# Kernel tuning notes

Hardware: AMD Instinct MI355X
Metric: run time of the kernel (lower is better)

The kernel has to match this reference:

```python
import jax, jax.numpy as jnp
import numpy as np

IN_DIM, EDGE_DIM, HID = 128, 64, 128
N_A, N_B, E_AB, E_AA = 50000, 50000, 320000, 320000


def setup_inputs() -> dict:
    key = jax.random.key(0)
    ks = jax.random.split(key, 13)
    inv = lambda n: 1.0 / np.sqrt(n)
    return {
        "x_a": jax.random.normal(ks[0], (N_A, IN_DIM), jnp.float32),
        "x_b": jax.random.normal(ks[1], (N_B, IN_DIM), jnp.float32),
        "ei_ab": jax.random.randint(ks[2], (2, E_AB), 0, N_A),
        "ea_ab": jax.random.normal(ks[3], (E_AB, EDGE_DIM), jnp.float32),
        "ei_aa": jax.random.randint(ks[4], (2, E_AA), 0, N_A),
        "ea_aa": jax.random.normal(ks[5], (E_AA, EDGE_DIM), jnp.float32),
        "Wh_w": jax.random.normal(ks[6], (EDGE_DIM, HID), jnp.float32) * inv(EDGE_DIM),
        "Wh_b": jnp.zeros((HID,), jnp.float32),
        "Wn_w": jax.random.normal(ks[7], (2 * IN_DIM, HID), jnp.float32) * inv(2 * IN_DIM),
        "Wn_b": jnp.zeros((HID,), jnp.float32),
        "w_e": jax.random.normal(ks[8], (HID,), jnp.float32) * inv(HID),
        "ft_w": jax.random.normal(ks[9], (IN_DIM, IN_DIM), jnp.float32) * inv(IN_DIM),
        "ft_b": jnp.zeros((IN_DIM,), jnp.float32),
    }


def reference(x_a, x_b, ei_ab, ea_ab, ei_aa, ea_aa,
              Wh_w, Wh_b, Wn_w, Wn_b, w_e, ft_w, ft_b):
    def edge_alpha(x_src, x_dst, ei, ea):
        # gather src/dst feats -> linear + relu -> score -> softmax over all edges
        s, d = ei[0], ei[1]
        nf = jnp.concatenate([x_src[s], x_dst[d]], axis=1)          # [E, 2*in_dim]
        h = jax.nn.relu(ea @ Wh_w + Wh_b + nf @ Wn_w + Wn_b)         # [E, hid]
        return jax.nn.softmax(h @ w_e, axis=0)                       # [E]

    alpha_ab = edge_alpha(x_a, x_b, ei_ab, ea_ab)
    alpha_aa = edge_alpha(x_a, x_a, ei_aa, ea_aa)

    lf_a = jnp.zeros_like(x_a)
    lf_b = jnp.zeros_like(x_b)
    s_ab, d_ab = ei_ab[0], ei_ab[1]
    # cross-type edge: scatter into both endpoint node types
    lf_a = lf_a.at[s_ab].add(-alpha_ab[:, None] * x_b[d_ab])
    lf_b = lf_b.at[d_ab].add(-alpha_ab[:, None] * x_a[s_ab])
    s_aa, d_aa = ei_aa[0], ei_aa[1]
    # same-type edge: single scatter (src side only, per original)
    lf_a = lf_a.at[s_aa].add(-alpha_aa[:, None] * x_a[d_aa])

    out_a = x_a + lf_a
    out_a = out_a + (out_a @ ft_w + ft_b)
    out_b = x_b + lf_b
    out_b = out_b + (out_b @ ft_w + ft_b)
    return out_a, out_b, alpha_ab, alpha_aa
```

## Files before the change

### kernel.cpp

```cpp
#include <hip/hip_runtime.h>
#include <hip/hip_fp16.h>
#include <cstdint>
#include <cstddef>

#define N_A   50000
#define N_B   50000
#define E_AB  320000
#define E_AA  320000
#define IN_DIM 128
#define HID    128
#define ED     64

using bf16x8 = __attribute__((ext_vector_type(8))) short;
using f32x4  = __attribute__((ext_vector_type(4))) float;
typedef unsigned short ushort_t;
typedef unsigned int   uint_t;

__device__ inline ushort_t bf16r(float f) {
    uint_t u = __float_as_uint(f);
    u = (u + 0x7FFF + ((u >> 16) & 1)) >> 16;
    return (ushort_t)u;
}
__device__ inline float bf2f(ushort_t h) {
    return __uint_as_float(((uint_t)h) << 16);
}
__device__ inline ushort_t f16r(float f) { return __half_as_ushort(__float2half_rn(f)); }
__device__ inline float f16f(ushort_t u) { return __half2float(__ushort_as_half(u)); }
__device__ inline uint_t packh2(float a, float b) {
    return (uint_t)f16r(a) | ((uint_t)f16r(b) << 16);
}

__device__ inline void online_merge(float& m, float& l, float om, float ol) {
    const float nm = fmaxf(m, om);
    l = l * __expf(m - nm) + ol * __expf(om - nm);
    m = nm;
}

__global__ __launch_bounds__(64) void prep_w_all(
    const float* __restrict__ Wh, const float* __restrict__ W1,
    const float* __restrict__ W2, const float* __restrict__ FT,
    const float* __restrict__ we,
    ushort_t* __restrict__ BhWh, ushort_t* __restrict__ BlWh,
    ushort_t* __restrict__ BhW1, ushort_t* __restrict__ BlW1,
    ushort_t* __restrict__ BhW2, ushort_t* __restrict__ BlW2,
    ushort_t* __restrict__ BhFT, ushort_t* __restrict__ BlFT,
    float* __restrict__ wep)
{
    const int f = blockIdx.x;
    const int lane = threadIdx.x;
    if (f == 112) {
#pragma unroll
        for (int q = 0; q < 2; ++q) {
            const int idx = lane + q * 64;
            const int l15 = idx >> 3, ct = idx & 7;
            wep[idx] = we[ct * 16 + l15];
        }
        return;
    }
    const float* W; ushort_t *oh, *ol; int KT, fl;
    if (f < 16)      { W = Wh; oh = BhWh; ol = BlWh; KT = 2; fl = f; }
    else if (f < 48) { W = W1; oh = BhW1; ol = BlW1; KT = 4; fl = f - 16; }
    else if (f < 80) { W = W2; oh = BhW2; ol = BlW2; KT = 4; fl = f - 48; }
    else             { W = FT; oh = BhFT; ol = BlFT; KT = 4; fl = f - 80; }
    const int ct = fl / KT, kt = fl % KT;
    const int col = ct * 16 + (lane & 15);
    const int kb  = kt * 32 + (lane >> 4) * 8;
#pragma unroll
    for (int j = 0; j < 8; ++j) {
        const float v = W[(kb + j) * 128 + col];
        const ushort_t h = bf16r(v);
        oh[(size_t)(fl * 64 + lane) * 8 + j] = h;
        ol[(size_t)(fl * 64 + lane) * 8 + j] = bf16r(v - bf2f(h));
    }
}

__global__ __launch_bounds__(256) void proj_dual_mfma(
    const float* __restrict__ X,
    const ushort_t* __restrict__ B1h, const ushort_t* __restrict__ B1l,
    const ushort_t* __restrict__ B2h, const ushort_t* __restrict__ B2l,
    const float* __restrict__ bh, const float* __restrict__ bn,
    ushort_t* __restrict__ P1, ushort_t* __restrict__ P2,
    ushort_t* __restrict__ X16, int N)
{
    const int lane = threadIdx.x & 63;
    const int l15 = lane & 15, lg = lane >> 4;
    const int r0 = blockIdx.x * 64 + (threadIdx.x >> 6) * 16;
    const int arow = (r0 + l15 < N) ? (r0 + l15) : (N - 1);

    bf16x8 ahi[4], alo[4];
#pragma unroll
    for (int kt = 0; kt < 4; ++kt) {
        float v[8];
        *(float4*)(v + 0) = *(const float4*)&X[(size_t)arow * 128 + kt * 32 + lg * 8];
        *(float4*)(v + 4) = *(const float4*)&X[(size_t)arow * 128 + kt * 32 + lg * 8 + 4];
        uint4 xu;
        xu.x = packh2(v[0], v[1]); xu.y = packh2(v[2], v[3]);
        xu.z = packh2(v[4], v[5]); xu.w = packh2(v[6], v[7]);
        *(uint4*)&X16[(size_t)arow * 128 + kt * 32 + lg * 8] = xu;
#pragma unroll
        for (int j = 0; j < 8; ++j) {
            const ushort_t h = bf16r(v[j]);
            ahi[kt][j] = (short)h;
            alo[kt][j] = (short)bf16r(v[j] - bf2f(h));
        }
    }

    f32x4 acc1[8], acc2[8];
#pragma unroll
    for (int ct = 0; ct < 8; ++ct) {
        const float b = bh[ct * 16 + l15] + bn[ct * 16 + l15];
        acc1[ct] = (f32x4){b, b, b, b};
        acc2[ct] = (f32x4){0.f, 0.f, 0.f, 0.f};
    }

#pragma unroll
    for (int ct = 0; ct < 8; ++ct) {
#pragma unroll
        for (int kt = 0; kt < 4; ++kt) {
            const size_t fo = (size_t)((ct * 4 + kt) * 64 + lane) * 8;
            const bf16x8 b1h = *(const bf16x8*)&B1h[fo];
            const bf16x8 b1l = *(const bf16x8*)&B1l[fo];
            const bf16x8 b2h = *(const bf16x8*)&B2h[fo];
            const bf16x8 b2l = *(const bf16x8*)&B2l[fo];
            acc1[ct] = __builtin_amdgcn_mfma_f32_16x16x32_bf16(ahi[kt], b1h, acc1[ct], 0, 0, 0);
            acc1[ct] = __builtin_amdgcn_mfma_f32_16x16x32_bf16(alo[kt], b1h, acc1[ct], 0, 0, 0);
            acc1[ct] = __builtin_amdgcn_mfma_f32_16x16x32_bf16(ahi[kt], b1l, acc1[ct], 0, 0, 0);
            acc2[ct] = __builtin_amdgcn_mfma_f32_16x16x32_bf16(ahi[kt], b2h, acc2[ct], 0, 0, 0);
            acc2[ct] = __builtin_amdgcn_mfma_f32_16x16x32_bf16(alo[kt], b2h, acc2[ct], 0, 0, 0);
            acc2[ct] = __builtin_amdgcn_mfma_f32_16x16x32_bf16(ahi[kt], b2l, acc2[ct], 0, 0, 0);
        }
    }
#pragma unroll
    for (int i = 0; i < 4; ++i) {
        const int row = r0 + lg * 4 + i;
        if (row < N) {
            uint4 u1, u2;
            u1.x = packh2(acc1[0][i], acc1[1][i]); u1.y = packh2(acc1[2][i], acc1[3][i]);
            u1.z = packh2(acc1[4][i], acc1[5][i]); u1.w = packh2(acc1[6][i], acc1[7][i]);
            u2.x = packh2(acc2[0][i], acc2[1][i]); u2.y = packh2(acc2[2][i], acc2[3][i]);
            u2.z = packh2(acc2[4][i], acc2[5][i]); u2.w = packh2(acc2[6][i], acc2[7][i]);
            *(uint4*)&P1[(size_t)row * 128 + l15 * 8] = u1;
            *(uint4*)&P2[(size_t)row * 128 + l15 * 8] = u2;
        }
    }
}

__global__ __launch_bounds__(256) void proj_single_mfma(
    const float* __restrict__ X,
    const ushort_t* __restrict__ Bh, const ushort_t* __restrict__ Bl,
    ushort_t* __restrict__ P, ushort_t* __restrict__ X16, int N)
{
    const int lane = threadIdx.x & 63;
    const int l15 = lane & 15, lg = lane >> 4;
    const int r0 = blockIdx.x * 64 + (threadIdx.x >> 6) * 16;
    const int arow = (r0 + l15 < N) ? (r0 + l15) : (N - 1);

    bf16x8 ahi[4], alo[4];
#pragma unroll
    for (int kt = 0; kt < 4; ++kt) {
        float v[8];
        *(float4*)(v + 0) = *(const float4*)&X[(size_t)arow * 128 + kt * 32 + lg * 8];
        *(float4*)(v + 4) = *(const float4*)&X[(size_t)arow * 128 + kt * 32 + lg * 8 + 4];
        uint4 xu;
        xu.x = packh2(v[0], v[1]); xu.y = packh2(v[2], v[3]);
        xu.z = packh2(v[4], v[5]); xu.w = packh2(v[6], v[7]);
        *(uint4*)&X16[(size_t)arow * 128 + kt * 32 + lg * 8] = xu;
#pragma unroll
        for (int j = 0; j < 8; ++j) {
            const ushort_t h = bf16r(v[j]);
            ahi[kt][j] = (short)h;
            alo[kt][j] = (short)bf16r(v[j] - bf2f(h));
        }
    }

    f32x4 acc[8];
#pragma unroll
    for (int ct = 0; ct < 8; ++ct) acc[ct] = (f32x4){0.f, 0.f, 0.f, 0.f};

#pragma unroll
    for (int ct = 0; ct < 8; ++ct) {
#pragma unroll
        for (int kt = 0; kt < 4; ++kt) {
            const size_t fo = (size_t)((ct * 4 + kt) * 64 + lane) * 8;
            const bf16x8 bhf = *(const bf16x8*)&Bh[fo];
            const bf16x8 blf = *(const bf16x8*)&Bl[fo];
            acc[ct] = __builtin_amdgcn_mfma_f32_16x16x32_bf16(ahi[kt], bhf, acc[ct], 0, 0, 0);
            acc[ct] = __builtin_amdgcn_mfma_f32_16x16x32_bf16(alo[kt], bhf, acc[ct], 0, 0, 0);
            acc[ct] = __builtin_amdgcn_mfma_f32_16x16x32_bf16(ahi[kt], blf, acc[ct], 0, 0, 0);
        }
    }
#pragma unroll
    for (int i = 0; i < 4; ++i) {
        const int row = r0 + lg * 4 + i;
        if (row < N) {
            uint4 u;
            u.x = packh2(acc[0][i], acc[1][i]); u.y = packh2(acc[2][i], acc[3][i]);
            u.z = packh2(acc[4][i], acc[5][i]); u.w = packh2(acc[6][i], acc[7][i]);
            *(uint4*)&P[(size_t)row * 128 + l15 * 8] = u;
        }
    }
}

__global__ __launch_bounds__(512) void edge_score_k(
    const float* __restrict__ ea_ab, const float* __restrict__ ea_aa,
    const int*   __restrict__ ei_ab, const int*   __restrict__ ei_aa,
    const ushort_t* __restrict__ P1h,
    const ushort_t* __restrict__ P2ah, const ushort_t* __restrict__ P2bh,
    const ushort_t* __restrict__ Bhi,  const ushort_t* __restrict__ Blo,
    const float* __restrict__ wep,
    float* __restrict__ scAB, float* __restrict__ scAA,
    int* __restrict__ cntA, int* __restrict__ cntB,
    int* __restrict__ rkAab, int* __restrict__ rkBab, int* __restrict__ rkAaa,
    float* __restrict__ pm, float* __restrict__ pl)
{
    const int t    = threadIdx.x;
    const int lane = t & 63;
    const int l15  = lane & 15;
    const int lg   = lane >> 4;
    const int wv   = t >> 6;
    const int type = (blockIdx.x >= 2500);
    const int bb   = type ? (blockIdx.x - 2500) : blockIdx.x;
    const int eb   = bb * 128;

    const float* __restrict__ ea  = type ? ea_aa : ea_ab;
    const int*   __restrict__ ei  = type ? ei_aa : ei_ab;
    const ushort_t* __restrict__ P2h = type ? P2ah : P2bh;
    float* __restrict__ score = type ? scAA : scAB;

    __shared__ ushort_t sBh[8192];
    __shared__ ushort_t sBl[8192];
    {
        const uint4* gh = (const uint4*)Bhi;
        const uint4* gl = (const uint4*)Blo;
        uint4* sh = (uint4*)sBh;
        uint4* sl = (uint4*)sBl;
#pragma unroll
        for (int i = 0; i < 2; ++i) {
            sh[t + i * 512] = gh[t + i * 512];
            sl[t + i * 512] = gl[t + i * 512];
        }
    }

    if (t < 128) {
        const int e = eb + t;
        const int s = ei[e];
        const int r = atomicAdd(&cntA[s], 1);
        if (type) rkAaa[e] = r; else rkAab[e] = r;
    } else if (t < 256 && !type) {
        const int e = eb + (t - 128);
        const int d = ei[(size_t)E_AB + e];
        rkBab[e] = atomicAdd(&cntB[d], 1);
    }

    const int e0 = eb + wv * 16;

    int sidx[4], didx[4];
#pragma unroll
    for (int i = 0; i < 4; ++i) {
        const int e = e0 + lg * 4 + i;
        sidx[i] = ei[e];
        didx[i] = ei[(size_t)E_AB + e];
    }
    uint4 p1u[4], p2u[4];
#pragma unroll
    for (int i = 0; i < 4; ++i) {
        p1u[i] = *(const uint4*)&P1h[(size_t)sidx[i] * 128 + l15 * 8];
        p2u[i] = *(const uint4*)&P2h[(size_t)didx[i] * 128 + l15 * 8];
    }

    const float* arow = &ea[(size_t)(e0 + l15) * 64 + lg * 8];
    float af[16];
    *(float4*)(af + 0)  = *(const float4*)(arow + 0);
    *(float4*)(af + 4)  = *(const float4*)(arow + 4);
    *(float4*)(af + 8)  = *(const float4*)(arow + 32);
    *(float4*)(af + 12) = *(const float4*)(arow + 36);

    bf16x8 ahi0, alo0, ahi1, alo1;
#pragma unroll
    for (int j = 0; j < 8; ++j) {
        const ushort_t h0 = bf16r(af[j]);
        ahi0[j] = (short)h0;
        alo0[j] = (short)bf16r(af[j] - bf2f(h0));
        const ushort_t h1 = bf16r(af[8 + j]);
        ahi1[j] = (short)h1;
        alo1[j] = (short)bf16r(af[8 + j] - bf2f(h1));
    }

    __syncthreads();

    f32x4 acc[8];
#pragma unroll
    for (int ct = 0; ct < 8; ++ct) acc[ct] = (f32x4){0.f, 0.f, 0.f, 0.f};

#pragma unroll
    for (int ct = 0; ct < 8; ++ct) {
        const bf16x8 bh0 = *(const bf16x8*)&sBh[(ct * 2 + 0) * 512 + lane * 8];
        const bf16x8 bl0 = *(const bf16x8*)&sBl[(ct * 2 + 0) * 512 + lane * 8];
        const bf16x8 bh1 = *(const bf16x8*)&sBh[(ct * 2 + 1) * 512 + lane * 8];
        const bf16x8 bl1 = *(const bf16x8*)&sBl[(ct * 2 + 1) * 512 + lane * 8];
        acc[ct] = __builtin_amdgcn_mfma_f32_16x16x32_bf16(ahi0, bh0, acc[ct], 0, 0, 0);
        acc[ct] = __builtin_amdgcn_mfma_f32_16x16x32_bf16(alo0, bh0, acc[ct], 0, 0, 0);
        acc[ct] = __builtin_amdgcn_mfma_f32_16x16x32_bf16(ahi0, bl0, acc[ct], 0, 0, 0);
        acc[ct] = __builtin_amdgcn_mfma_f32_16x16x32_bf16(ahi1, bh1, acc[ct], 0, 0, 0);
        acc[ct] = __builtin_amdgcn_mfma_f32_16x16x32_bf16(alo1, bh1, acc[ct], 0, 0, 0);
        acc[ct] = __builtin_amdgcn_mfma_f32_16x16x32_bf16(ahi1, bl1, acc[ct], 0, 0, 0);
    }

    float w8[8];
    *(float4*)(w8 + 0) = *(const float4*)&wep[l15 * 8];
    *(float4*)(w8 + 4) = *(const float4*)&wep[l15 * 8 + 4];

    float part[4];
#pragma unroll
    for (int i = 0; i < 4; ++i) {
        const __half2* h1 = (const __half2*)&p1u[i];
        const __half2* h2 = (const __half2*)&p2u[i];
        float p = 0.f;
#pragma unroll
        for (int q = 0; q < 4; ++q) {
            const float2 pf = __half22float2(__hadd2(h1[q], h2[q]));
            p = fmaf(fmaxf(acc[2 * q][i] + pf.x, 0.f), w8[2 * q], p);
            p = fmaf(fmaxf(acc[2 * q + 1][i] + pf.y, 0.f), w8[2 * q + 1], p);
        }
        part[i] = p;
    }
#pragma unroll
    for (int m = 8; m >= 1; m >>= 1) {
#pragma unroll
        for (int i = 0; i < 4; ++i) part[i] += __shfl_xor(part[i], m, 64);
    }
    if (l15 == 0) {
#pragma unroll
        for (int i = 0; i < 4; ++i) score[e0 + lg * 4 + i] = part[i];
    }

    float mw = fmaxf(fmaxf(part[0], part[1]), fmaxf(part[2], part[3]));
    float lw = __expf(part[0] - mw) + __expf(part[1] - mw)
             + __expf(part[2] - mw) + __expf(part[3] - mw);
#pragma unroll
    for (int off = 16; off <= 32; off <<= 1) {
        const float om = __shfl_xor(mw, off, 64);
        const float ol = __shfl_xor(lw, off, 64);
        online_merge(mw, lw, om, ol);
    }
    __shared__ float smm[8], sll[8];
    if (lane == 0) { smm[wv] = mw; sll[wv] = lw; }
    __syncthreads();
    if (t == 0) {
        float M = smm[0], L = sll[0];
        for (int i = 1; i < 8; ++i) online_merge(M, L, smm[i], sll[i]);
        pm[blockIdx.x] = M;
        pl[blockIdx.x] = L;
    }
}

__global__ __launch_bounds__(1024) void softmax_final_kernel(
    const float* __restrict__ pm, const float* __restrict__ pl,
    float* __restrict__ ML, int nPart)
{
    const int type = blockIdx.x;
    const float* mi = pm + type * nPart;
    const float* li = pl + type * nPart;
    float m = -1e30f, l = 0.f;
    for (int i = threadIdx.x; i < nPart; i += 1024) online_merge(m, l, mi[i], li[i]);
#pragma unroll
    for (int off = 1; off < 64; off <<= 1) {
        const float om = __shfl_xor(m, off, 64);
        const float ol = __shfl_xor(l, off, 64);
        online_merge(m, l, om, ol);
    }
    __shared__ float smm[16], sll[16];
    const int w = threadIdx.x >> 6, lane = threadIdx.x & 63;
    if (lane == 0) { smm[w] = m; sll[w] = l; }
    __syncthreads();
    if (threadIdx.x == 0) {
        float M = smm[0], L = sll[0];
        for (int i = 1; i < 16; ++i) online_merge(M, L, smm[i], sll[i]);
        ML[type * 2]     = M;
        ML[type * 2 + 1] = L;
    }
}

__global__ __launch_bounds__(1024) void csr_scan_kernel(
    const int* __restrict__ cntA, int* __restrict__ offA,
    const int* __restrict__ cntB, int* __restrict__ offB, int N)
{
    const int* cnt = (blockIdx.x == 0) ? cntA : cntB;
    int* off = (blockIdx.x == 0) ? offA : offB;

    __shared__ int warpsum[16];
    const int t = threadIdx.x, lane = t & 63, w = t >> 6;
    int carry = 0;

    for (int base = 0; base < N; base += 1024) {
        const int i = base + t;
        const int v = (i < N) ? cnt[i] : 0;
        int x = v;
#pragma unroll
        for (int d = 1; d < 64; d <<= 1) {
            const int y = __shfl_up(x, d, 64);
            if (lane >= d) x += y;
        }
        if (lane == 63) warpsum[w] = x;
        __syncthreads();
        if (w == 0 && lane < 16) {
            int s = warpsum[lane];
#pragma unroll
            for (int d = 1; d < 16; d <<= 1) {
                const int y = __shfl_up(s, d, 64);
                if (lane >= d) s += y;
            }
            warpsum[lane] = s;
        }
        __syncthreads();
        const int excl = (x - v) + ((w > 0) ? warpsum[w - 1] : 0) + carry;
        if (i < N) off[i] = excl;
        carry += warpsum[15];
        __syncthreads();
    }
    if (t == 0) off[N] = carry;
}

__global__ __launch_bounds__(256) void csr_fill_kernel(
    const int* __restrict__ ei_ab, const int* __restrict__ ei_aa,
    float* __restrict__ scAB, float* __restrict__ scAA,
    const float* __restrict__ ML,
    const int* __restrict__ offA, const int* __restrict__ offB,
    const int* __restrict__ rkAab, const int* __restrict__ rkBab,
    const int* __restrict__ rkAaa,
    int2* __restrict__ idxA, int2* __restrict__ idxB)
{
    const int i = blockIdx.x * 256 + threadIdx.x;
    const float Mab = ML[0], rLab = 1.0f / ML[1];
    const float Maa = ML[2], rLaa = 1.0f / ML[3];
    if (i < E_AB) {
        const float a = __expf(scAB[i] - Mab) * rLab;
        scAB[i] = a;
        const int s = ei_ab[i], d = ei_ab[E_AB + i];
        const int ab = __float_as_int(a);
        int pA = offA[s] + rkAab[i]; if (pA > 2 * E_AB - 1) pA = 2 * E_AB - 1;
        int pB = offB[d] + rkBab[i]; if (pB > E_AB - 1) pB = E_AB - 1;
        idxA[pA] = make_int2(d | (1 << 20), ab);
        idxB[pB] = make_int2(s, ab);
    }
    if (i < E_AA) {
        const float a = __expf(scAA[i] - Maa) * rLaa;
        scAA[i] = a;
        const int s = ei_aa[i];
        const int daa = ei_aa[E_AA + i];
        int pA = offA[s] + rkAaa[i]; if (pA > 2 * E_AB - 1) pA = 2 * E_AB - 1;
        idxA[pA] = make_int2(daa, __float_as_int(a));
    }
}

__global__ __launch_bounds__(256) void gather_final(
    const int*  __restrict__ off, const int2* __restrict__ idx,
    const ushort_t* __restrict__ xa16, const ushort_t* __restrict__ xb16,
    const float* __restrict__ xself,
    const ushort_t* __restrict__ Bh, const ushort_t* __restrict__ Bl,
    const float* __restrict__ fb,
    float* __restrict__ T, int N)
{
    const int lane = threadIdx.x & 63;
    const int l15  = lane & 15, lg = lane >> 4;
    const int wv   = threadIdx.x >> 6;
    const int r0   = blockIdx.x * 64 + wv * 16;

    for (int s = 0; s < 4; ++s) {
        const int row = r0 + s * 4 + lg;
        if (row < N) {
            const int beg = off[row], end = off[row + 1];
            float a8[8];
            *(float4*)(a8 + 0) = *(const float4*)&xself[(size_t)row * 128 + l15 * 8];
            *(float4*)(a8 + 4) = *(const float4*)&xself[(size_t)row * 128 + l15 * 8 + 4];
            int e = beg;
            for (; e + 3 < end; e += 4) {
                int2 q[4];
#pragma unroll
                for (int k = 0; k < 4; ++k) q[k] = idx[e + k];
                uint4 f[4];
#pragma unroll
                for (int k = 0; k < 4; ++k) {
                    const ushort_t* sp = (q[k].x & (1 << 20)) ? xb16 : xa16;
                    f[k] = *(const uint4*)&sp[(size_t)(q[k].x & 0xFFFFF) * 128 + l15 * 8];
                }
#pragma unroll
                for (int k = 0; k < 4; ++k) {
                    const float al = __int_as_float(q[k].y);
                    const __half2* hp = (const __half2*)&f[k];
#pragma unroll
                    for (int j = 0; j < 4; ++j) {
                        const float2 vf = __half22float2(hp[j]);
                        a8[2 * j]     = fmaf(-al, vf.x, a8[2 * j]);
                        a8[2 * j + 1] = fmaf(-al, vf.y, a8[2 * j + 1]);
                    }
                }
            }
            for (; e < end; ++e) {
                const int2 q0 = idx[e];
                const float al = __int_as_float(q0.y);
                const ushort_t* sp = (q0.x & (1 << 20)) ? xb16 : xa16;
                const uint4 f0 = *(const uint4*)&sp[(size_t)(q0.x & 0xFFFFF) * 128 + l15 * 8];
                const __half2* hp = (const __half2*)&f0;
#pragma unroll
                for (int j = 0; j < 4; ++j) {
                    const float2 vf = __half22float2(hp[j]);
                    a8[2 * j]     = fmaf(-al, vf.x, a8[2 * j]);
                    a8[2 * j + 1] = fmaf(-al, vf.y, a8[2 * j + 1]);
                }
            }
            *(float4*)&T[(size_t)row * 128 + l15 * 8]     = *(float4*)(a8 + 0);
            *(float4*)&T[(size_t)row * 128 + l15 * 8 + 4] = *(float4*)(a8 + 4);
        }
    }
    __syncthreads();

    const int arow = (r0 + l15 < N) ? (r0 + l15) : (N - 1);
    bf16x8 ahi[4], alo[4];
#pragma unroll
    for (int kt = 0; kt < 4; ++kt) {
        float v[8];
        *(float4*)(v + 0) = *(const float4*)&T[(size_t)arow * 128 + kt * 32 + lg * 8];
        *(float4*)(v + 4) = *(const float4*)&T[(size_t)arow * 128 + kt * 32 + lg * 8 + 4];
#pragma unroll
        for (int j = 0; j < 8; ++j) {
            const ushort_t h = bf16r(v[j]);
            ahi[kt][j] = (short)h;
            alo[kt][j] = (short)bf16r(v[j] - bf2f(h));
        }
    }

    f32x4 acc[8];
#pragma unroll
    for (int ct = 0; ct < 8; ++ct) {
        const float b = fb[ct * 16 + l15];
#pragma unroll
        for (int i = 0; i < 4; ++i) {
            const int row = r0 + lg * 4 + i;
            const int rr = (row < N) ? row : (N - 1);
            acc[ct][i] = T[(size_t)rr * 128 + ct * 16 + l15] + b;
        }
    }

#pragma unroll
    for (int ct = 0; ct < 8; ++ct) {
#pragma unroll
        for (int kt = 0; kt < 4; ++kt) {
            const size_t fo = (size_t)((ct * 4 + kt) * 64 + lane) * 8;
            const bf16x8 bhf = *(const bf16x8*)&Bh[fo];
            const bf16x8 blf = *(const bf16x8*)&Bl[fo];
            acc[ct] = __builtin_amdgcn_mfma_f32_16x16x32_bf16(ahi[kt], bhf, acc[ct], 0, 0, 0);
            acc[ct] = __builtin_amdgcn_mfma_f32_16x16x32_bf16(alo[kt], bhf, acc[ct], 0, 0, 0);
            acc[ct] = __builtin_amdgcn_mfma_f32_16x16x32_bf16(ahi[kt], blf, acc[ct], 0, 0, 0);
        }
    }
#pragma unroll
    for (int ct = 0; ct < 8; ++ct) {
#pragma unroll
        for (int i = 0; i < 4; ++i) {
            const int row = r0 + lg * 4 + i;
            if (row < N) T[(size_t)row * 128 + ct * 16 + l15] = acc[ct][i];
        }
    }
}

extern "C" void kernel_launch(void* const* d_in, const int* in_sizes, int n_in,
                              void* d_out, int out_size, void* d_ws, size_t ws_size,
                              hipStream_t stream)
{
    const float* x_a   = (const float*)d_in[0];
    const float* x_b   = (const float*)d_in[1];
    const int*   ei_ab = (const int*)d_in[2];
    const float* ea_ab = (const float*)d_in[3];
    const int*   ei_aa = (const int*)d_in[4];
    const float* ea_aa = (const float*)d_in[5];
    const float* Wh_w  = (const float*)d_in[6];
    const float* Wh_b  = (const float*)d_in[7];
    const float* Wn_w  = (const float*)d_in[8];
    const float* Wn_b  = (const float*)d_in[9];
    const float* w_e   = (const float*)d_in[10];
    const float* ft_w  = (const float*)d_in[11];
    const float* ft_b  = (const float*)d_in[12];

    float* out = (float*)d_out;
    float* ws  = (float*)d_ws;

    ushort_t* P1h  = (ushort_t*)(ws);
    ushort_t* P2ah = (ushort_t*)(ws + 3200000);
    ushort_t* P2bh = (ushort_t*)(ws + 6400000);
    ushort_t* xa16 = (ushort_t*)(ws + 9600000);
    ushort_t* xb16 = (ushort_t*)(ws + 12800000);
    int* rkAab = (int*)(ws + 16000000);
    int* rkBab = (int*)(ws + 16320000);
    int* rkAaa = (int*)(ws + 16640000);
    int* cntA  = (int*)(ws + 16960000);
    int* cntB  = (int*)(ws + 17010000);
    int* offA  = (int*)(ws + 17060000);
    int* offB  = (int*)(ws + 17110004);
    float* pm  = ws + 17160008;
    float* pl  = ws + 17165008;
    float* ML  = ws + 17170008;
    float* wep = ws + 17170016;
    ushort_t* FR = (ushort_t*)(ws + 17170208);
    ushort_t* BhWh = FR;
    ushort_t* BlWh = FR + 8192;
    ushort_t* BhW1 = FR + 16384;
    ushort_t* BlW1 = FR + 32768;
    ushort_t* BhW2 = FR + 49152;
    ushort_t* BlW2 = FR + 65536;
    ushort_t* BhFT = FR + 81920;
    ushort_t* BlFT = FR + 98304;
    int2* idxA = (int2*)(ws + 17240000);
    int2* idxB = (int2*)(ws + 18520000);

    float* TA   = out;
    float* TB   = out + 6400000;
    float* alAB = out + 12800000;
    float* alAA = out + 13120000;

    hipMemsetAsync(cntA, 0, 100000 * sizeof(int), stream);
    prep_w_all<<<113, 64, 0, stream>>>(Wh_w, Wn_w, Wn_w + 128 * 128, ft_w, w_e,
                                       BhWh, BlWh, BhW1, BlW1, BhW2, BlW2, BhFT, BlFT, wep);

    proj_dual_mfma<<<(N_A + 63) / 64, 256, 0, stream>>>(x_a, BhW1, BlW1, BhW2, BlW2,
                                                        Wh_b, Wn_b, P1h, P2ah, xa16, N_A);
    proj_single_mfma<<<(N_B + 63) / 64, 256, 0, stream>>>(x_b, BhW2, BlW2, P2bh, xb16, N_B);

    edge_score_k<<<5000, 512, 0, stream>>>(ea_ab, ea_aa, ei_ab, ei_aa,
                                           P1h, P2ah, P2bh, BhWh, BlWh, wep,
                                           alAB, alAA, cntA, cntB,
                                           rkAab, rkBab, rkAaa, pm, pl);

    softmax_final_kernel<<<2, 1024, 0, stream>>>(pm, pl, ML, 2500);

    csr_scan_kernel<<<2, 1024, 0, stream>>>(cntA, offA, cntB, offB, N_A);
    csr_fill_kernel<<<(E_AB + 255) / 256, 256, 0, stream>>>(ei_ab, ei_aa, alAB, alAA, ML,
                                                            offA, offB, rkAab, rkBab, rkAaa,
                                                            idxA, idxB);

    gather_final<<<(N_A + 63) / 64, 256, 0, stream>>>(offA, idxA, xa16, xb16, x_a,
                                                      BhFT, BlFT, ft_b, TA, N_A);
    gather_final<<<(N_B + 63) / 64, 256, 0, stream>>>(offB, idxB, xa16, xb16, x_b,
                                                      BhFT, BlFT, ft_b, TB, N_B);

    (void)in_sizes; (void)n_in; (void)out_size; (void)ws_size;
}
```

Before: 333.2 us.

## Halve edge-score LDS, emit per-wave softmax partials, and defer rank atomics

```diff
diff --git a/kernel.cpp b/kernel.cpp
--- a/kernel.cpp
+++ b/kernel.cpp
@@ -201,7 +201,7 @@
     }
 }
 
-__global__ __launch_bounds__(512) void edge_score_k(
+__global__ __launch_bounds__(512, 8) void edge_score_k(
     const float* __restrict__ ea_ab, const float* __restrict__ ea_aa,
     const int*   __restrict__ ei_ab, const int*   __restrict__ ei_aa,
     const ushort_t* __restrict__ P1h,
@@ -221,6 +221,7 @@
     const int type = (blockIdx.x >= 2500);
     const int bb   = type ? (blockIdx.x - 2500) : blockIdx.x;
     const int eb   = bb * 128;
+    const int gw   = blockIdx.x * 8 + wv;
 
     const float* __restrict__ ea  = type ? ea_aa : ea_ab;
     const int*   __restrict__ ei  = type ? ei_aa : ei_ab;
@@ -228,18 +229,102 @@
     float* __restrict__ score = type ? scAA : scAB;
 
     __shared__ ushort_t sBh[8192];
-    __shared__ ushort_t sBl[8192];
     {
         const uint4* gh = (const uint4*)Bhi;
-        const uint4* gl = (const uint4*)Blo;
         uint4* sh = (uint4*)sBh;
-        uint4* sl = (uint4*)sBl;
-#pragma unroll
-        for (int i = 0; i < 2; ++i) {
-            sh[t + i * 512] = gh[t + i * 512];
-            sl[t + i * 512] = gl[t + i * 512];
-        }
-    }
+        sh[t]       = gh[t];
+        sh[t + 512] = gh[t + 512];
+    }
+
+    const int e0 = eb + wv * 16;
+
+    const int4 sv = *(const int4*)&ei[e0 + lg * 4];
+    const int4 dv = *(const int4*)&ei[(size_t)E_AB + e0 + lg * 4];
+    const int sidx[4] = {sv.x, sv.y, sv.z, sv.w};
+    const int didx[4] = {dv.x, dv.y, dv.z, dv.w};
+    uint4 p1u[4], p2u[4];
+#pragma unroll
+    for (int i = 0; i < 4; ++i) {
+        p1u[i] = *(const uint4*)&P1h[(size_t)sidx[i] * 128 + l15 * 8];
+        p2u[i] = *(const uint4*)&P2h[(size_t)didx[i] * 128 + l15 * 8];
+    }
+
+    float w8[8];
+    *(float4*)(w8 + 0) = *(const float4*)&wep[l15 * 8];
+    *(float4*)(w8 + 4) = *(const float4*)&wep[l15 * 8 + 4];
+
+    const float* arow = &ea[(size_t)(e0 + l15) * 64 + lg * 8];
+    float af[16];
+    *(float4*)(af + 0)  = *(const float4*)(arow + 0);
+    *(float4*)(af + 4)  = *(const float4*)(arow + 4);
+    *(float4*)(af + 8)  = *(const float4*)(arow + 32);
+    *(float4*)(af + 12) = *(const float4*)(arow + 36);
+
+    bf16x8 ahi0, alo0, ahi1, alo1;
+#pragma unroll
+    for (int j = 0; j < 8; ++j) {
+        const ushort_t h0 = bf16r(af[j]);
+        ahi0[j] = (short)h0;
+        alo0[j] = (short)bf16r(af[j] - bf2f(h0));
+        const ushort_t h1 = bf16r(af[8 + j]);
+        ahi1[j] = (short)h1;
+        alo1[j] = (short)bf16r(af[8 + j] - bf2f(h1));
+    }
+
+    __syncthreads();
+
+    f32x4 acc[8];
+#pragma unroll
+    for (int ct = 0; ct < 8; ++ct) acc[ct] = (f32x4){0.f, 0.f, 0.f, 0.f};
+
+#pragma unroll
+    for (int ct = 0; ct < 8; ++ct) {
+        const bf16x8 bh0 = *(const bf16x8*)&sBh[(ct * 2 + 0) * 512 + lane * 8];
+        const bf16x8 bh1 = *(const bf16x8*)&sBh[(ct * 2 + 1) * 512 + lane * 8];
+        const bf16x8 bl0 = *(const bf16x8*)&Blo[(size_t)(ct * 2 + 0) * 512 + lane * 8];
+        const bf16x8 bl1 = *(const bf16x8*)&Blo[(size_t)(ct * 2 + 1) * 512 + lane * 8];
+        acc[ct] = __builtin_amdgcn_mfma_f32_16x16x32_bf16(ahi0, bh0, acc[ct], 0, 0, 0);
+        acc[ct] = __builtin_amdgcn_mfma_f32_16x16x32_bf16(alo0, bh0, acc[ct], 0, 0, 0);
+        acc[ct] = __builtin_amdgcn_mfma_f32_16x16x32_bf16(ahi0, bl0, acc[ct], 0, 0, 0);
+        acc[ct] = __builtin_amdgcn_mfma_f32_16x16x32_bf16(ahi1, bh1, acc[ct], 0, 0, 0);
+        acc[ct] = __builtin_amdgcn_mfma_f32_16x16x32_bf16(alo1, bh1, acc[ct], 0, 0, 0);
+        acc[ct] = __builtin_amdgcn_mfma_f32_16x16x32_bf16(ahi1, bl1, acc[ct], 0, 0, 0);
+    }
+
+    float part[4];
+#pragma unroll
+    for (int i = 0; i < 4; ++i) {
+        const __half2* h1 = (const __half2*)&p1u[i];
+        const __half2* h2 = (const __half2*)&p2u[i];
+        float p = 0.f;
+#pragma unroll
+        for (int q = 0; q < 4; ++q) {
+            const float2 pf = __half22float2(__hadd2(h1[q], h2[q]));
+            p = fmaf(fmaxf(acc[2 * q][i] + pf.x, 0.f), w8[2 * q], p);
+            p = fmaf(fmaxf(acc[2 * q + 1][i] + pf.y, 0.f), w8[2 * q + 1], p);
+        }
+        part[i] = p;
+    }
+#pragma unroll
+    for (int m = 8; m >= 1; m >>= 1) {
+#pragma unroll
+        for (int i = 0; i < 4; ++i) part[i] += __shfl_xor(part[i], m, 64);
+    }
+    if (l15 == 0) {
+#pragma unroll
+        for (int i = 0; i < 4; ++i) score[e0 + lg * 4 + i] = part[i];
+    }
+
+    float mw = fmaxf(fmaxf(part[0], part[1]), fmaxf(part[2], part[3]));
+    float lw = __expf(part[0] - mw) + __expf(part[1] - mw)
+             + __expf(part[2] - mw) + __expf(part[3] - mw);
+#pragma unroll
+    for (int off = 16; off <= 32; off <<= 1) {
+        const float om = __shfl_xor(mw, off, 64);
+        const float ol = __shfl_xor(lw, off, 64);
+        online_merge(mw, lw, om, ol);
+    }
+    if (lane == 0) { pm[gw] = mw; pl[gw] = lw; }
 
     if (t < 128) {
         const int e = eb + t;
@@ -250,107 +335,6 @@
         const int e = eb + (t - 128);
         const int d = ei[(size_t)E_AB + e];
         rkBab[e] = atomicAdd(&cntB[d], 1);
-    }
-
-    const int e0 = eb + wv * 16;
-
-    int sidx[4], didx[4];
-#pragma unroll
-    for (int i = 0; i < 4; ++i) {
-        const int e = e0 + lg * 4 + i;
-        sidx[i] = ei[e];
-        didx[i] = ei[(size_t)E_AB + e];
-    }
-    uint4 p1u[4], p2u[4];
-#pragma unroll
-    for (int i = 0; i < 4; ++i) {
-        p1u[i] = *(const uint4*)&P1h[(size_t)sidx[i] * 128 + l15 * 8];
-        p2u[i] = *(const uint4*)&P2h[(size_t)didx[i] * 128 + l15 * 8];
-    }
-
-    const float* arow = &ea[(size_t)(e0 + l15) * 64 + lg * 8];
-    float af[16];
-    *(float4*)(af + 0)  = *(const float4*)(arow + 0);
-    *(float4*)(af + 4)  = *(const float4*)(arow + 4);
-    *(float4*)(af + 8)  = *(const float4*)(arow + 32);
-    *(float4*)(af + 12) = *(const float4*)(arow + 36);
-
-    bf16x8 ahi0, alo0, ahi1, alo1;
-#pragma unroll
-    for (int j = 0; j < 8; ++j) {
-        const ushort_t h0 = bf16r(af[j]);
-        ahi0[j] = (short)h0;
-        alo0[j] = (short)bf16r(af[j] - bf2f(h0));
-        const ushort_t h1 = bf16r(af[8 + j]);
-        ahi1[j] = (short)h1;
-        alo1[j] = (short)bf16r(af[8 + j] - bf2f(h1));
-    }
-
-    __syncthreads();
-
-    f32x4 acc[8];
-#pragma unroll
-    for (int ct = 0; ct < 8; ++ct) acc[ct] = (f32x4){0.f, 0.f, 0.f, 0.f};
-
-#pragma unroll
-    for (int ct = 0; ct < 8; ++ct) {
-        const bf16x8 bh0 = *(const bf16x8*)&sBh[(ct * 2 + 0) * 512 + lane * 8];
-        const bf16x8 bl0 = *(const bf16x8*)&sBl[(ct * 2 + 0) * 512 + lane * 8];
-        const bf16x8 bh1 = *(const bf16x8*)&sBh[(ct * 2 + 1) * 512 + lane * 8];
-        const bf16x8 bl1 = *(const bf16x8*)&sBl[(ct * 2 + 1) * 512 + lane * 8];
-        acc[ct] = __builtin_amdgcn_mfma_f32_16x16x32_bf16(ahi0, bh0, acc[ct], 0, 0, 0);
-        acc[ct] = __builtin_amdgcn_mfma_f32_16x16x32_bf16(alo0, bh0, acc[ct], 0, 0, 0);
-        acc[ct] = __builtin_amdgcn_mfma_f32_16x16x32_bf16(ahi0, bl0, acc[ct], 0, 0, 0);
-        acc[ct] = __builtin_amdgcn_mfma_f32_16x16x32_bf16(ahi1, bh1, acc[ct], 0, 0, 0);
-        acc[ct] = __builtin_amdgcn_mfma_f32_16x16x32_bf16(alo1, bh1, acc[ct], 0, 0, 0);
-        acc[ct] = __builtin_amdgcn_mfma_f32_16x16x32_bf16(ahi1, bl1, acc[ct], 0, 0, 0);
-    }
-
-    float w8[8];
-    *(float4*)(w8 + 0) = *(const float4*)&wep[l15 * 8];
-    *(float4*)(w8 + 4) = *(const float4*)&wep[l15 * 8 + 4];
-
-    float part[4];
-#pragma unroll
-    for (int i = 0; i < 4; ++i) {
-        const __half2* h1 = (const __half2*)&p1u[i];
-        const __half2* h2 = (const __half2*)&p2u[i];
-        float p = 0.f;
-#pragma unroll
-        for (int q = 0; q < 4; ++q) {
-            const float2 pf = __half22float2(__hadd2(h1[q], h2[q]));
-            p = fmaf(fmaxf(acc[2 * q][i] + pf.x, 0.f), w8[2 * q], p);
-            p = fmaf(fmaxf(acc[2 * q + 1][i] + pf.y, 0.f), w8[2 * q + 1], p);
-        }
-        part[i] = p;
-    }
-#pragma unroll
-    for (int m = 8; m >= 1; m >>= 1) {
-#pragma unroll
-        for (int i = 0; i < 4; ++i) part[i] += __shfl_xor(part[i], m, 64);
-    }
-    if (l15 == 0) {
-#pragma unroll
-        for (int i = 0; i < 4; ++i) score[e0 + lg * 4 + i] = part[i];
-    }
-
-    float mw = fmaxf(fmaxf(part[0], part[1]), fmaxf(part[2], part[3]));
-    float lw = __expf(part[0] - mw) + __expf(part[1] - mw)
-             + __expf(part[2] - mw) + __expf(part[3] - mw);
-#pragma unroll
-    for (int off = 16; off <= 32; off <<= 1) {
-        const float om = __shfl_xor(mw, off, 64);
-        const float ol = __shfl_xor(lw, off, 64);
-        online_merge(mw, lw, om, ol);
-    }
-    __shared__ float smm[8], sll[8];
-    if (lane == 0) { smm[wv] = mw; sll[wv] = lw; }
-    __syncthreads();
-    if (t == 0) {
-        float M = smm[0], L = sll[0];
-        for (int i = 1; i < 8; ++i) online_merge(M, L, smm[i], sll[i]);
-        pm[blockIdx.x] = M;
-        pl[blockIdx.x] = L;
     }
 }
 
@@ -598,10 +582,10 @@
     int* offA  = (int*)(ws + 17060000);
     int* offB  = (int*)(ws + 17110004);
     float* pm  = ws + 17160008;
-    float* pl  = ws + 17165008;
-    float* ML  = ws + 17170008;
-    float* wep = ws + 17170016;
-    ushort_t* FR = (ushort_t*)(ws + 17170208);
+    float* pl  = ws + 17200008;
+    float* ML  = ws + 17240008;
+    float* wep = ws + 17240016;
+    ushort_t* FR = (ushort_t*)(ws + 17240208);
     ushort_t* BhWh = FR;
     ushort_t* BlWh = FR + 8192;
     ushort_t* BhW1 = FR + 16384;
@@ -610,8 +594,8 @@
     ushort_t* BlW2 = FR + 65536;
     ushort_t* BhFT = FR + 81920;
     ushort_t* BlFT = FR + 98304;
-    int2* idxA = (int2*)(ws + 17240000);
-    int2* idxB = (int2*)(ws + 18520000);
+    int2* idxA = (int2*)(ws + 17300000);
+    int2* idxB = (int2*)(ws + 18580000);
 
     float* TA   = out;
     float* TB   = out + 6400000;
@@ -631,7 +615,7 @@
                                            alAB, alAA, cntA, cntB,
                                            rkAab, rkBab, rkAaa, pm, pl);
 
-    softmax_final_kernel<<<2, 1024, 0, stream>>>(pm, pl, ML, 2500);
+    softmax_final_kernel<<<2, 1024, 0, stream>>>(pm, pl, ML, 20000);
 
     csr_scan_kernel<<<2, 1024, 0, stream>>>(cntA, offA, cntB, offB, N_A);
     csr_fill_kernel<<<(E_AB + 255) / 256, 256, 0, stream>>>(ei_ab, ei_aa, alAB, alAA, ML,
```

Measured after the change: 522.6 us. 1.57x slower.
